# Performance work log

Hardware: AMD Instinct MI355X
Metric: run time of the kernel (lower is better)

## Reference

```python
import jax, jax.numpy as jnp
import numpy as np

BLOCK = 128
FP8_MAX = 448.0


def _quant_weight(w):
    # Per 128x128 block quantization to fp8 e4m3, matching weight.scale layout [N/128, K/128].
    N, K = w.shape
    nb, kb = N // BLOCK, K // BLOCK
    wb = w.reshape(nb, BLOCK, kb, BLOCK)
    s = jnp.max(jnp.abs(wb), axis=(1, 3)) / FP8_MAX  # [nb, kb]
    q = (wb / s[:, None, :, None]).astype(jnp.float8_e4m3fn).astype(jnp.float32)
    return q.reshape(N, K), s


def setup_inputs() -> dict:
    key = jax.random.key(0)
    kx, kw = jax.random.split(key)
    M, K, N = 4096, 4096, 4096
    x = jax.random.normal(kx, (M, K), dtype=jnp.float32)
    w = jax.random.normal(kw, (N, K), dtype=jnp.float32) * 0.02
    w_q, w_s = _quant_weight(w)
    return {"x": x, "w_q": w_q, "w_s": w_s}


def _act_quant(x):
    # Per-row, per-128-element block quantization (act_quant kernel): s = max|x|/448, y = fp8(x/s).
    M, K = x.shape
    kb = K // BLOCK
    xb = x.reshape(M, kb, BLOCK)
    s = jnp.max(jnp.abs(xb), axis=-1) / FP8_MAX  # [M, kb]
    q = (xb / s[..., None]).astype(jnp.float8_e4m3fn).astype(jnp.float32)
    return q.reshape(M, K), s


def reference(x, w_q, w_s):
    # fp8 GEMM with inline block-wise dequant (fp32 accumulation): since the scales are
    # constant within each K-block, accumulating (A_blk @ B_blk^T) * a_s * b_s over blocks
    # equals dequantizing both operands elementwise then one fp32 matmul.
    M, K = x.shape
    N = w_q.shape[0]
    nb, kb = N // BLOCK, K // BLOCK
    x_q, x_s = _act_quant(x)
    a = x_q.reshape(M, kb, BLOCK) * x_s[..., None]                       # dequant activations
    a = a.reshape(M, K)
    b = (w_q.reshape(nb, BLOCK, kb, BLOCK) * w_s[:, None, :, None]).reshape(N, K)  # dequant weights
    return a @ b.T  # [M, N]
```

## Files before the change

kernel.cpp:

```cpp
#include <hip/hip_runtime.h>

typedef float f32x4 __attribute__((ext_vector_type(4)));
typedef int   i32x4 __attribute__((ext_vector_type(4)));
typedef int   i32x8 __attribute__((ext_vector_type(8)));

#define FP8_MAX 448.0f
#define AS1 __attribute__((address_space(1)))
#define AS3 __attribute__((address_space(3)))

__global__ __launch_bounds__(256) void act_quant_k(const float* __restrict__ x,
                                                   unsigned char* __restrict__ xq,
                                                   float* __restrict__ xst,
                                                   int M, int K) {
    const int t   = threadIdx.x;
    const int qb  = blockIdx.x * 8 + (t >> 5);
    const int l32 = t & 31;
    const int row = qb >> 5;
    const int kb  = qb & 31;
    const size_t base = (size_t)row * K + (size_t)kb * 128 + (size_t)l32 * 4;

    float4 v = *(const float4*)(x + base);
    float am = fmaxf(fmaxf(fabsf(v.x), fabsf(v.y)), fmaxf(fabsf(v.z), fabsf(v.w)));
#pragma unroll
    for (int off = 1; off < 32; off <<= 1)
        am = fmaxf(am, __shfl_xor(am, off, 64));

    const float s = am / FP8_MAX;
    const float q0 = v.x / s, q1 = v.y / s, q2 = v.z / s, q3 = v.w / s;
    int p = __builtin_amdgcn_cvt_pk_fp8_f32(q0, q1, 0, false);
    p     = __builtin_amdgcn_cvt_pk_fp8_f32(q2, q3, p, true);

    const int klo = l32 << 2;
    const size_t abyte = (((size_t)(row >> 4) * 32 + kb) << 11)
                       + ((klo >> 5) << 9) + ((row & 15) << 5) + (klo & 31);
    *(int*)(xq + abyte) = p;
    if (l32 == 0) xst[(size_t)kb * M + row] = s;
}

__global__ __launch_bounds__(256) void wq_cvt_k(const float* __restrict__ w,
                                                unsigned char* __restrict__ wq) {
    const size_t i = ((size_t)blockIdx.x * 256 + threadIdx.x) * 4;
    float4 v = *(const float4*)(w + i);
    int p = __builtin_amdgcn_cvt_pk_fp8_f32(v.x, v.y, 0, false);
    p     = __builtin_amdgcn_cvt_pk_fp8_f32(v.z, v.w, p, true);
    *(int*)(wq + i) = p;
}

__global__ __launch_bounds__(256, 2) void gemm_fp8_blk(
    const unsigned char* __restrict__ Aq,
    const unsigned char* __restrict__ Bq,
    const float* __restrict__ xst,
    const float* __restrict__ wsc,
    float* __restrict__ C, int M, int N, int K) {
    __shared__ unsigned char Bs[2][16384];
    __shared__ float Ss[2][128];

    const int t    = threadIdx.x;
    const int lane = t & 63;
    const int wave = t >> 6;
    const int wr   = wave >> 1;
    const int wc   = wave & 1;
    const int bm   = blockIdx.y * 128;
    const int bn   = blockIdx.x * 128;

    const int srow   = t >> 3;
    const int scolsw = (((t & 7) ^ ((t >> 3) & 7)) << 4);
    const unsigned char* gB = Bq + (size_t)(bn + srow) * K + scolsw;
    const float* gS = xst + bm + ((wave & 1) << 6) + lane;
    const int ldsoff = wave << 10;
    const int sSoff  = (wave & 1) << 8;

    const int r15 = lane & 15;
    const int g   = lane >> 4;
    const int km  = r15 & 7;
    const int pc0 = (((2 * g) ^ km) << 4);
    const int pc1 = pc0 ^ 16;
    const int bBase = (wc * 64 + r15) << 7;
    const int ssB   = wr * 64 + (g << 2);

    const unsigned char* gA0 = Aq + (((size_t)(bm >> 4) + wr * 4) << 16) + (lane << 5);

    const float* wscp = wsc + ((bn >> 7) << 5);

#define STG_B(BUF, KB, I)                                                       \
    __builtin_amdgcn_global_load_lds(                                           \
        (const AS1 void*)(gB + (size_t)(I) * 32 * K + ((size_t)(KB) << 7)),     \
        (AS3 void*)(&Bs[BUF][0] + (I) * 4096 + ldsoff), 16, 0, 0)
#define STG_S(KB)                                                               \
    __builtin_amdgcn_global_load_lds(                                           \
        (const AS1 void*)(gS + (size_t)(KB) * M),                               \
        (AS3 void*)((unsigned char*)&Ss[(KB) & 1][0] + sSoff), 4, 0, 0)
#define VMCNT0() asm volatile("s_waitcnt vmcnt(0)" ::: "memory")

#define RDB8(RB) ({                                                             \
    i32x4 lo_ = *(const i32x4*)(bp + (RB) + pc0);                               \
    i32x4 hi_ = *(const i32x4*)(bp + (RB) + pc1);                               \
    __builtin_shufflevector(lo_, hi_, 0, 1, 2, 3, 4, 5, 6, 7); })
#define RDA8(PTR) ({                                                            \
    i32x4 lo_ = *(const i32x4*)(PTR);                                           \
    i32x4 hi_ = *(const i32x4*)((PTR) + 16);                                    \
    __builtin_shufflevector(lo_, hi_, 0, 1, 2, 3, 4, 5, 6, 7); })

    f32x4 accM[4][4] = {};
    const f32x4 z4 = {0.f, 0.f, 0.f, 0.f};

    STG_S(0);
#pragma unroll
    for (int i = 0; i < 4; ++i) STG_B(0, 0, i);
    VMCNT0();
    __builtin_amdgcn_s_barrier();
    asm volatile("" ::: "memory");

#pragma unroll 1
    for (int kb = 0; kb < 32; ++kb) {
        const int buf = kb & 1;
        const float wsv = wscp[kb];
        const unsigned char* bp = &Bs[buf][0];
        const float* sp = &Ss[buf][0];
        const unsigned char* apg = gA0 + ((size_t)kb << 11);

        i32x8 pa[4];
#pragma unroll
        for (int m = 0; m < 4; ++m) pa[m] = RDA8(apg + (m << 16));

        i32x8 pb[4];
        f32x4 sc[4];
#pragma unroll
        for (int n = 0; n < 4; ++n) pb[n] = RDB8(bBase + (n << 11));
#pragma unroll
        for (int m = 0; m < 4; ++m)
            sc[m] = (*(const f32x4*)(sp + ssB + (m << 4))) * wsv;

        if (kb < 31) {
            STG_S(kb + 1);
#pragma unroll
            for (int i = 0; i < 4; ++i) STG_B(buf ^ 1, kb + 1, i);
        }

        __builtin_amdgcn_s_setprio(1);
        f32x4 q[4][4];
#pragma unroll
        for (int m = 0; m < 4; ++m)
#pragma unroll
            for (int n = 0; n < 4; ++n)
                q[m][n] = __builtin_amdgcn_mfma_scale_f32_16x16x128_f8f6f4(
                    pa[m], pb[n], z4, 0, 0,
                    0, 0x7F7F7F7F,
                    0, 0x7F7F7F7F);
        __builtin_amdgcn_s_setprio(0);
#pragma unroll
        for (int m = 0; m < 4; ++m)
#pragma unroll
            for (int n = 0; n < 4; ++n)
                accM[m][n] += q[m][n] * sc[m];

        VMCNT0();
        __builtin_amdgcn_s_barrier();
        asm volatile("" ::: "memory");
    }

    const int cm = bm + wr * 64 + (g << 2);
    const int cn = bn + wc * 64 + r15;
#pragma unroll
    for (int m = 0; m < 4; ++m)
#pragma unroll
        for (int n = 0; n < 4; ++n) {
            float* cp = C + (size_t)(cm + m * 16) * N + (cn + n * 16);
#pragma unroll
            for (int r = 0; r < 4; ++r) cp[(size_t)r * N] = accM[m][n][r];
        }
#undef STG_B
#undef STG_S
#undef VMCNT0
#undef RDB8
#undef RDA8
}

extern "C" void kernel_launch(void* const* d_in, const int* in_sizes, int n_in,
                              void* d_out, int out_size, void* d_ws, size_t ws_size,
                              hipStream_t stream) {
    const float* x   = (const float*)d_in[0];
    const float* wqf = (const float*)d_in[1];
    const float* wsc = (const float*)d_in[2];
    float* out = (float*)d_out;

    const int M = 4096, N = 4096, K = 4096;

    unsigned char* xq  = (unsigned char*)d_ws;
    unsigned char* wq8 = (unsigned char*)d_ws + (size_t)M * K;
    float* xst = (float*)((unsigned char*)d_ws + (size_t)M * K + (size_t)N * K);

    act_quant_k<<<M * (K / 128) / 8, 256, 0, stream>>>(x, xq, xst, M, K);
    wq_cvt_k<<<(N / 4) * (K / 256), 256, 0, stream>>>(wqf, wq8);
    dim3 grid(N / 128, M / 128);
    gemm_fp8_blk<<<grid, 256, 0, stream>>>(xq, wq8, xst, wsc, out, M, N, K);
}
```

Baseline: 116.9 us.

## Prefetch next A fragments into registers and relax vmcnt wait in GEMM loop

The GEMM main loop is unrolled by two, with ping-pong register buffers for the A operand. The next k-block's A fragments are loaded from global memory one iteration early, issued after the LDS staging loads for B and scales. The end-of-iteration wait becomes vmcnt(8), so the A register prefetch can stay in flight across the barrier while the LDS-bound loads complete. This aims to hide global A-load latency behind MFMA work, at the cost of more live registers, which could hurt occupancy at two blocks per CU.

```diff
diff --git a/kernel.cpp b/kernel.cpp
--- a/kernel.cpp
+++ b/kernel.cpp
@@ -90,7 +90,6 @@
     __builtin_amdgcn_global_load_lds(                                           \
         (const AS1 void*)(gS + (size_t)(KB) * M),                               \
         (AS3 void*)((unsigned char*)&Ss[(KB) & 1][0] + sSoff), 4, 0, 0)
-#define VMCNT0() asm volatile("s_waitcnt vmcnt(0)" ::: "memory")
 
 #define RDB8(RB) ({                                                             \
     i32x4 lo_ = *(const i32x4*)(bp + (RB) + pc0);                               \
@@ -101,62 +100,66 @@
     i32x4 hi_ = *(const i32x4*)((PTR) + 16);                                    \
     __builtin_shufflevector(lo_, hi_, 0, 1, 2, 3, 4, 5, 6, 7); })
 
+#define STEPX(BUF, PCUR, PNXT, KB, LAST) do {                                   \
+    const float wsv = wscp[KB];                                                 \
+    const unsigned char* bp = &Bs[BUF][0];                                      \
+    const float* sp = &Ss[BUF][0];                                              \
+    if (!(LAST)) {                                                              \
+        STG_S((KB) + 1);                                                        \
+        _Pragma("unroll")                                                       \
+        for (int i = 0; i < 4; ++i) STG_B((BUF) ^ 1, (KB) + 1, i);              \
+        __builtin_amdgcn_sched_barrier(0);   \
+        const unsigned char* apn = gA0 + ((size_t)((KB) + 1) << 11);            \
+        _Pragma("unroll")                                                       \
+        for (int m = 0; m < 4; ++m) PNXT[m] = RDA8(apn + (m << 16));            \
+    }                                                                           \
+    i32x8 pb[4]; f32x4 sc[4];                                                   \
+    _Pragma("unroll")                                                           \
+    for (int n = 0; n < 4; ++n) pb[n] = RDB8(bBase + (n << 11));                \
+    _Pragma("unroll")                                                           \
+    for (int m = 0; m < 4; ++m)                                                 \
+        sc[m] = (*(const f32x4*)(sp + ssB + (m << 4))) * wsv;                   \
+    __builtin_amdgcn_s_setprio(1);                                              \
+    f32x4 q[4][4];                                                              \
+    _Pragma("unroll")                                                           \
+    for (int m = 0; m < 4; ++m)                                                 \
+        _Pragma("unroll")                                                       \
+        for (int n = 0; n < 4; ++n)                                             \
+            q[m][n] = __builtin_amdgcn_mfma_scale_f32_16x16x128_f8f6f4(         \
+                PCUR[m], pb[n], z4, 0, 0,                                       \
+                0, 0x7F7F7F7F,                    \
+                0, 0x7F7F7F7F);                              \
+    __builtin_amdgcn_s_setprio(0);                                              \
+    _Pragma("unroll")                                                           \
+    for (int m = 0; m < 4; ++m)                                                 \
+        _Pragma("unroll")                                                       \
+        for (int n = 0; n < 4; ++n)                                             \
+            accM[m][n] += q[m][n] * sc[m];                                      \
+    if (!(LAST)) {                                                              \
+        asm volatile("s_waitcnt vmcnt(8)" ::: "memory");     \
+        __builtin_amdgcn_s_barrier();                                           \
+        asm volatile("" ::: "memory");                                          \
+    }                                                                           \
+} while (0)
+
     f32x4 accM[4][4] = {};
     const f32x4 z4 = {0.f, 0.f, 0.f, 0.f};
+    i32x8 paA[4], paB[4];
 
     STG_S(0);
 #pragma unroll
     for (int i = 0; i < 4; ++i) STG_B(0, 0, i);
-    VMCNT0();
+#pragma unroll
+    for (int m = 0; m < 4; ++m) paA[m] = RDA8(gA0 + (m << 16));
+    asm volatile("s_waitcnt vmcnt(0)" ::: "memory");
     __builtin_amdgcn_s_barrier();
     asm volatile("" ::: "memory");
 
 #pragma unroll 1
-    for (int kb = 0; kb < 32; ++kb) {
-        const int buf = kb & 1;
-        const float wsv = wscp[kb];
-        const unsigned char* bp = &Bs[buf][0];
-        const float* sp = &Ss[buf][0];
-        const unsigned char* apg = gA0 + ((size_t)kb << 11);
-
-        i32x8 pa[4];
-#pragma unroll
-        for (int m = 0; m < 4; ++m) pa[m] = RDA8(apg + (m << 16));
-
-        i32x8 pb[4];
-        f32x4 sc[4];
-#pragma unroll
-        for (int n = 0; n < 4; ++n) pb[n] = RDB8(bBase + (n << 11));
-#pragma unroll
-        for (int m = 0; m < 4; ++m)
-            sc[m] = (*(const f32x4*)(sp + ssB + (m << 4))) * wsv;
-
-        if (kb < 31) {
-            STG_S(kb + 1);
-#pragma unroll
-            for (int i = 0; i < 4; ++i) STG_B(buf ^ 1, kb + 1, i);
-        }
-
-        __builtin_amdgcn_s_setprio(1);
-        f32x4 q[4][4];
-#pragma unroll
-        for (int m = 0; m < 4; ++m)
-#pragma unroll
-            for (int n = 0; n < 4; ++n)
-                q[m][n] = __builtin_amdgcn_mfma_scale_f32_16x16x128_f8f6f4(
-                    pa[m], pb[n], z4, 0, 0,
-                    0, 0x7F7F7F7F,
-                    0, 0x7F7F7F7F);
-        __builtin_amdgcn_s_setprio(0);
-#pragma unroll
-        for (int m = 0; m < 4; ++m)
-#pragma unroll
-            for (int n = 0; n < 4; ++n)
-                accM[m][n] += q[m][n] * sc[m];
-
-        VMCNT0();
-        __builtin_amdgcn_s_barrier();
-        asm volatile("" ::: "memory");
+    for (int kbp = 0; kbp < 16; ++kbp) {
+        const int kb0 = kbp << 1;
+        STEPX(0, paA, paB, kb0, 0);
+        STEPX(1, paB, paA, kb0 + 1, (kbp == 15));
     }
 
     const int cm = bm + wr * 64 + (g << 2);
@@ -171,9 +174,9 @@
         }
 #undef STG_B
 #undef STG_S
-#undef VMCNT0
 #undef RDB8
 #undef RDA8
+#undef STEPX
 }
 
 extern "C" void kernel_launch(void* const* d_in, const int* in_sizes, int n_in,
```

Result: slower. 396.5 us (+239.3%).
